# Kernel optimization log

Measured on AMD Instinct MI355X. Metric: run time of the kernel, lower is better.

The kernel has to match this reference:

```python
import jax, jax.numpy as jnp
import numpy as np

NUM_RBF = 16
MAX_REL = 32
TOP_K = 48
RBF_D_MIN, RBF_D_MAX = 2.0, 22.0
CB_A, CB_B, CB_C = -0.58273431, 0.56802827, -0.54067466
LN_EPS = 1e-5


def gather_L(x, idx):
    # x: (B, L, ...)  idx: (B, L, K) -> (B, L, K, ...): neighbors along L per batch
    return jax.vmap(lambda xb, ib: xb[ib])(x, idx)


def rbf_encode(D):
    mu = jnp.linspace(RBF_D_MIN, RBF_D_MAX, NUM_RBF, dtype=D.dtype)  # (16,)
    sigma = (RBF_D_MAX - RBF_D_MIN) / NUM_RBF
    return jnp.exp(-((D[..., None] - mu) / sigma) ** 2)


def setup_inputs() -> dict:
    key = jax.random.key(0)
    ks = jax.random.split(key, 4)
    B, L = 4, 2048
    num_pos, hidden = 16, 128
    X = jax.random.normal(ks[0], (B, L, 4, 3), jnp.float32) * 3.0
    residue_mask = jnp.ones((B, L), jnp.float32)
    R_idx = jnp.tile(jnp.arange(L, dtype=jnp.int32)[None, :], (B, 1))
    chain_labels = jnp.zeros((B, L), jnp.int32)
    W_pos = jax.random.normal(ks[1], (2 * MAX_REL + 2, num_pos), jnp.float32) * 0.1
    b_pos = jnp.zeros((num_pos,), jnp.float32)
    W_edge = jax.random.normal(ks[2], (25 * NUM_RBF + num_pos, hidden), jnp.float32) * 0.05
    ln_gamma = jnp.ones((hidden,), jnp.float32)
    ln_beta = jnp.zeros((hidden,), jnp.float32)
    return dict(X=X, residue_mask=residue_mask, R_idx=R_idx, chain_labels=chain_labels,
                W_pos=W_pos, b_pos=b_pos, W_edge=W_edge, ln_gamma=ln_gamma, ln_beta=ln_beta)


def reference(X, residue_mask, R_idx, chain_labels, W_pos, b_pos, W_edge, ln_gamma, ln_beta):
    B, L = X.shape[:2]
    # virtual CB from N, CA, C
    N, CA, C = X[..., 0, :], X[..., 1, :], X[..., 2, :]
    b = CA - N
    c = C - CA
    a = jnp.cross(b, c)
    CB = CB_A * a + CB_B * b + CB_C * c + CA                      # (B, L, 3)
    atoms_5 = jnp.concatenate([X, CB[:, :, None, :]], axis=-2)    # (B, L, 5, 3)

    # kNN on CA-CA squared distances, masked columns pushed far away
    diff = CA[:, :, None, :] - CA[:, None, :, :]                  # (B, L, L, 3)
    dist_sq = jnp.sum(diff ** 2, axis=-1)
    dist_sq = dist_sq + (1.0 - residue_mask)[:, None, :] * 1e6
    _, E_idx = jax.lax.top_k(-dist_sq, TOP_K)                     # smallest-k -> (B, L, K)

    # 25 atom-pair RBF features
    X_g = gather_L(atoms_5, E_idx)                                # (B, L, K, 5, 3)
    D = jnp.sqrt(jnp.sum((atoms_5[:, :, None, :, None, :]
                          - X_g[:, :, :, None, :, :]) ** 2, axis=-1) + 1e-6)  # (B,L,K,5,5)
    rbf = rbf_encode(D).reshape(B, L, TOP_K, 25 * NUM_RBF)        # (B, L, K, 400)

    # positional encodings (ProteinMPNN style)
    R_g = gather_L(R_idx, E_idx)                                  # (B, L, K)
    C_g = gather_L(chain_labels, E_idx)
    offset = R_idx[:, :, None] - R_g
    same_chain = (chain_labels[:, :, None] == C_g).astype(jnp.int32)
    d = jnp.clip(offset + MAX_REL, 0, 2 * MAX_REL) * same_chain + (1 - same_chain) * (2 * MAX_REL + 1)
    d_onehot = jax.nn.one_hot(d, 2 * MAX_REL + 2, dtype=W_pos.dtype)  # (B, L, K, 66)
    pos_enc = jnp.einsum('blkc,cp->blkp', d_onehot, W_pos) + b_pos    # (B, L, K, 16)

    edge_input = jnp.concatenate([pos_enc, rbf], axis=-1)         # (B, L, K, 416)
    E = jnp.einsum('blkc,ch->blkh', edge_input, W_edge)           # (B, L, K, 128)
    mean = jnp.mean(E, axis=-1, keepdims=True)
    var = jnp.var(E, axis=-1, keepdims=True)
    E = (E - mean) * jax.lax.rsqrt(var + LN_EPS) * ln_gamma + ln_beta
    return E_idx, E
```

## Files before the change

kernel.cpp:

```cpp
#include <hip/hip_runtime.h>
#include <hip/hip_bf16.h>

#define BB 4
#define LL 2048
#define KK 48
#define HH 128
#define CANDCAP 384
#define FSTR 40
#define DLT 1.06666666667f

using bf16x8 = __attribute__((ext_vector_type(8))) short;
using f32x4  = __attribute__((ext_vector_type(4))) float;
using u64x2  = __attribute__((ext_vector_type(2))) unsigned long long;

__global__ __launch_bounds__(256) void pf13_prep_w(
    const float* __restrict__ Wedge, const float* __restrict__ Wpos,
    const float* __restrict__ bpos, short* __restrict__ Wt) {
    int idx = blockIdx.x * 256 + threadIdx.x;
    if (idx >= 16 * 8 * 16 * 32) return;
    int j  = idx & 7;
    int kg = (idx >> 3) & 3;
    int col = (idx >> 5) & 15;
    int nt = (idx >> 9) & 7;
    int kt = idx >> 12;
    int k = kt * 32 + kg * 8 + j;
    int n = nt * 16 + col;
    float v = 0.0f;
    if (kt < 13) {
        if (k < 400) v = Wedge[(size_t)(16 + k) * HH + n];
    } else {
        int d = k - 416;
        if (d < 66) {
            float s = 0.f;
            #pragma unroll
            for (int p = 0; p < 16; ++p)
                s += (Wpos[d * 16 + p] + bpos[p]) * Wedge[p * HH + n];
            v = s;
        }
    }
    __hip_bfloat16 h = __float2bfloat16(v);
    Wt[idx] = *reinterpret_cast<short*>(&h);
}

__global__ __launch_bounds__(256) void pf13_prep_ca(const float* __restrict__ X,
                                                    const float* __restrict__ mask,
                                                    float4* __restrict__ caq) {
    int i = blockIdx.x * 256 + threadIdx.x;
    if (i >= BB * LL) return;
    const float* x = X + (size_t)i * 12;
    float bias = __fmul_rn(1.0f - mask[i], 1.0e6f);
    caq[i] = make_float4(x[3], x[4], x[5], bias);
}

__global__ __launch_bounds__(256, 6) void pf13_main(
    const float* __restrict__ X,
    const int* __restrict__ Ridx, const int* __restrict__ chain,
    const float* __restrict__ gamma, const float* __restrict__ beta,
    const short* __restrict__ Wt, const float4* __restrict__ caq,
    float* __restrict__ outIdx, float* __restrict__ outEdge) {

    const int row = blockIdx.x;
    const int bq = row >> 11, lq = row & (LL - 1);
    const int tid = threadIdx.x;
    const int lane = tid & 63, wid = tid >> 6;
    const float* Xb = X + (size_t)bq * LL * 12;
    const float4* caqb = caq + (size_t)bq * LL;

    __shared__ __align__(16) union {
        int hist[1024];
        unsigned long long cand[CANDCAP];
        float geo[KK * 15 + 16];
    } uA;
    __shared__ float sD[KK * 25];
    __shared__ __align__(16) short sFeat[2][KK * FSTR];
    __shared__ float sGB[2 * HH];
    __shared__ float sPartS[KK][4], sPartSS[KK][4];
    __shared__ float sMean[KK], sInv[KK];
    __shared__ int sSel[KK], sDcode[KK];
    __shared__ int sWsum[4];
    __shared__ int sBstar, sCc;

    if (tid < HH) { sGB[tid * 2] = gamma[tid]; sGB[tid * 2 + 1] = beta[tid]; }

    const float4 sc = caqb[lq];
    float dval[8];
    #pragma unroll
    for (int i = 0; i < 8; ++i) {
        float4 q = caqb[i * 256 + tid];
        float dx = __fadd_rn(sc.x, -q.x);
        float dy = __fadd_rn(sc.y, -q.y);
        float dz = __fadd_rn(sc.z, -q.z);
        float d2 = __fadd_rn(__fadd_rn(__fmul_rn(dx, dx), __fmul_rn(dy, dy)),
                             __fmul_rn(dz, dz));
        dval[i] = __fadd_rn(d2, q.w);
    }

    *reinterpret_cast<int4*>(&uA.hist[tid * 4]) = make_int4(0, 0, 0, 0);
    if (tid == 0) sCc = 0;
    __syncthreads();
    #pragma unroll
    for (int i = 0; i < 8; ++i)
        atomicAdd(&uA.hist[__float_as_uint(dval[i]) >> 22], 1);
    __syncthreads();

    int c0 = uA.hist[tid * 4 + 0];
    int c1 = uA.hist[tid * 4 + 1];
    int c2 = uA.hist[tid * 4 + 2];
    int c3 = uA.hist[tid * 4 + 3];
    int local = c0 + c1 + c2 + c3;
    int v = local;
    #pragma unroll
    for (int off = 1; off < 64; off <<= 1) {
        int o = __shfl_up(v, off, 64);
        if (lane >= off) v += o;
    }
    if (lane == 63) sWsum[wid] = v;
    __syncthreads();
    int woff = 0;
    #pragma unroll
    for (int w2 = 0; w2 < 4; ++w2) if (w2 < wid) woff += sWsum[w2];
    int incl = woff + v, excl = incl - local;
    if (excl < KK && incl >= KK) {
        int cum = excl, b = tid * 4;
        if (cum + c0 >= KK) sBstar = b;
        else { cum += c0;
            if (cum + c1 >= KK) sBstar = b + 1;
            else { cum += c1;
                if (cum + c2 >= KK) sBstar = b + 2;
                else sBstar = b + 3; } }
    }
    __syncthreads();

    int bstar = sBstar;
    #pragma unroll
    for (int i = 0; i < 8; ++i) {
        unsigned int kb = __float_as_uint(dval[i]);
        if ((int)(kb >> 22) <= bstar) {
            int pos = atomicAdd(&sCc, 1);
            if (pos < CANDCAP)
                uA.cand[pos] =
                    ((unsigned long long)kb << 32) | (unsigned)(i * 256 + tid);
        }
    }
    __syncthreads();

    int C = sCc < CANDCAP ? sCc : CANDCAP;
    for (int ci = tid; ci < C; ci += 256) {
        unsigned long long me = uA.cand[ci];
        int rank = 0, j2 = 0;
        int Cv = C & ~7;
        for (; j2 < Cv; j2 += 8) {
            u64x2 q0 = *reinterpret_cast<u64x2*>(&uA.cand[j2]);
            u64x2 q1 = *reinterpret_cast<u64x2*>(&uA.cand[j2 + 2]);
            u64x2 q2 = *reinterpret_cast<u64x2*>(&uA.cand[j2 + 4]);
            u64x2 q3 = *reinterpret_cast<u64x2*>(&uA.cand[j2 + 6]);
            rank += (q0[0] < me) + (q0[1] < me) + (q1[0] < me) + (q1[1] < me)
                  + (q2[0] < me) + (q2[1] < me) + (q3[0] < me) + (q3[1] < me);
        }
        for (; j2 < C; ++j2) rank += (uA.cand[j2] < me) ? 1 : 0;
        if (rank < KK) sSel[rank] = (int)(me & 0xFFFFFFFFu);
    }
    __syncthreads();

    if (tid < KK) outIdx[(size_t)row * KK + tid] = (float)sSel[tid];

    const float KA = -0.58273431f, KB2 = 0.56802827f, KC = -0.54067466f;
    if (tid < KK) {
        int j = sSel[tid];
        const float* x = Xb + (size_t)j * 12;
        float u0 = x[3] - x[0], u1 = x[4] - x[1], u2 = x[5] - x[2];
        float w0 = x[6] - x[3], w1 = x[7] - x[4], w2 = x[8] - x[5];
        float r0 = u1 * w2 - u2 * w1;
        float r1 = u2 * w0 - u0 * w2;
        float r2 = u0 * w1 - u1 * w0;
        float* o = &uA.geo[tid * 15];
        #pragma unroll
        for (int t = 0; t < 12; ++t) o[t] = x[t];
        o[12] = KA * r0 + KB2 * u0 + KC * w0 + x[3];
        o[13] = KA * r1 + KB2 * u1 + KC * w1 + x[4];
        o[14] = KA * r2 + KB2 * u2 + KC * w2 + x[5];
        int offr = Ridx[row] - Ridx[(size_t)bq * LL + j];
        int same = (chain[row] == chain[(size_t)bq * LL + j]);
        int d = offr + 32;
        d = d < 0 ? 0 : (d > 64 ? 64 : d);
        sDcode[tid] = same ? d : 65;
    }
    if (tid == 64) {
        const float* x = Xb + (size_t)lq * 12;
        float u0 = x[3] - x[0], u1 = x[4] - x[1], u2 = x[5] - x[2];
        float w0 = x[6] - x[3], w1 = x[7] - x[4], w2 = x[8] - x[5];
        float r0 = u1 * w2 - u2 * w1;
        float r1 = u2 * w0 - u0 * w2;
        float r2 = u0 * w1 - u1 * w0;
        float* s = &uA.geo[720];
        #pragma unroll
        for (int t = 0; t < 12; ++t) s[t] = x[t];
        s[12] = KA * r0 + KB2 * u0 + KC * w0 + x[3];
        s[13] = KA * r1 + KB2 * u1 + KC * w1 + x[4];
        s[14] = KA * r2 + KB2 * u2 + KC * w2 + x[5];
    }
    __syncthreads();

    for (int idx = tid; idx < KK * 25; idx += 256) {
        int k = idx / 25, pq = idx % 25, p = pq / 5, q = pq % 5;
        float dx = uA.geo[720 + p * 3 + 0] - uA.geo[k * 15 + q * 3 + 0];
        float dy = uA.geo[720 + p * 3 + 1] - uA.geo[k * 15 + q * 3 + 1];
        float dz = uA.geo[720 + p * 3 + 2] - uA.geo[k * 15 + q * 3 + 2];
        sD[idx] = sqrtf(dx * dx + dy * dy + dz * dz + 1e-6f);
    }
    __syncthreads();

    auto feat_compute = [&](int kt, int fb) {
        if (tid < 192) {
            int pair = tid >> 1, half = tid & 1;
            int k = pair >> 1, pq_lo = pair & 1;
            int pq = kt * 2 + pq_lo;
            bf16x8 ov;
            if (pq < 25) {
                float Dv = sD[k * 25 + pq];
                float t0 = (Dv - 2.0f) * 0.8f;
                float tm = __builtin_fmaf(-(float)(half << 3), DLT, t0);
                #pragma unroll
                for (int mi = 0; mi < 8; ++mi) {
                    float val = __expf(-tm * tm);
                    __hip_bfloat16 hb = __float2bfloat16(val);
                    ov[mi] = *reinterpret_cast<short*>(&hb);
                    tm -= DLT;
                }
            } else {
                #pragma unroll
                for (int mi = 0; mi < 8; ++mi) ov[mi] = 0;
            }
            *reinterpret_cast<bf16x8*>(
                &sFeat[fb][k * FSTR + pq_lo * 16 + (half << 3)]) = ov;
        }
    };

    feat_compute(0, 0);
    __syncthreads();

    f32x4 acc[3][2];
    #pragma unroll
    for (int mt = 0; mt < 3; ++mt)
        #pragma unroll
        for (int nb = 0; nb < 2; ++nb) acc[mt][nb] = (f32x4){0.f, 0.f, 0.f, 0.f};
    const int nt0 = wid * 2;
    const int arow = lane & 15, kg = lane >> 4;

    int cur = 0;
    #pragma unroll 1
    for (int kt = 0; kt < 13; ++kt) {
        const short* wp = Wt + (((size_t)(kt * 8 + nt0) * 16 + arow) * 32 + kg * 8);
        bf16x8 b0 = *reinterpret_cast<const bf16x8*>(wp);
        bf16x8 b1 = *reinterpret_cast<const bf16x8*>(wp + 16 * 32);
        if (kt + 1 < 13) feat_compute(kt + 1, cur ^ 1);
        bf16x8 a0 = *reinterpret_cast<const bf16x8*>(&sFeat[cur][(arow     ) * FSTR + kg * 8]);
        bf16x8 a1 = *reinterpret_cast<const bf16x8*>(&sFeat[cur][(arow + 16) * FSTR + kg * 8]);
        bf16x8 a2 = *reinterpret_cast<const bf16x8*>(&sFeat[cur][(arow + 32) * FSTR + kg * 8]);
        acc[0][0] = __builtin_amdgcn_mfma_f32_16x16x32_bf16(a0, b0, acc[0][0], 0, 0, 0);
        acc[1][0] = __builtin_amdgcn_mfma_f32_16x16x32_bf16(a1, b0, acc[1][0], 0, 0, 0);
        acc[2][0] = __builtin_amdgcn_mfma_f32_16x16x32_bf16(a2, b0, acc[2][0], 0, 0, 0);
        acc[0][1] = __builtin_amdgcn_mfma_f32_16x16x32_bf16(a0, b1, acc[0][1], 0, 0, 0);
        acc[1][1] = __builtin_amdgcn_mfma_f32_16x16x32_bf16(a1, b1, acc[1][1], 0, 0, 0);
        acc[2][1] = __builtin_amdgcn_mfma_f32_16x16x32_bf16(a2, b1, acc[2][1], 0, 0, 0);
        if (kt + 1 < 13) { __syncthreads(); cur ^= 1; }
    }

    int dc0 = sDcode[arow], dc1 = sDcode[arow + 16], dc2 = sDcode[arow + 32];
    #pragma unroll 1
    for (int kp = 0; kp < 3; ++kp) {
        int base = kp * 32 + kg * 8;
        bf16x8 a0, a1, a2;
        #pragma unroll
        for (int j = 0; j < 8; ++j) {
            a0[j] = (dc0 == base + j) ? (short)0x3F80 : (short)0;
            a1[j] = (dc1 == base + j) ? (short)0x3F80 : (short)0;
            a2[j] = (dc2 == base + j) ? (short)0x3F80 : (short)0;
        }
        const short* wp = Wt + (((size_t)((13 + kp) * 8 + nt0) * 16 + arow) * 32 + kg * 8);
        bf16x8 b0 = *reinterpret_cast<const bf16x8*>(wp);
        bf16x8 b1 = *reinterpret_cast<const bf16x8*>(wp + 16 * 32);
        acc[0][0] = __builtin_amdgcn_mfma_f32_16x16x32_bf16(a0, b0, acc[0][0], 0, 0, 0);
        acc[1][0] = __builtin_amdgcn_mfma_f32_16x16x32_bf16(a1, b0, acc[1][0], 0, 0, 0);
        acc[2][0] = __builtin_amdgcn_mfma_f32_16x16x32_bf16(a2, b0, acc[2][0], 0, 0, 0);
        acc[0][1] = __builtin_amdgcn_mfma_f32_16x16x32_bf16(a0, b1, acc[0][1], 0, 0, 0);
        acc[1][1] = __builtin_amdgcn_mfma_f32_16x16x32_bf16(a1, b1, acc[1][1], 0, 0, 0);
        acc[2][1] = __builtin_amdgcn_mfma_f32_16x16x32_bf16(a2, b1, acc[2][1], 0, 0, 0);
    }

    #pragma unroll
    for (int mt = 0; mt < 3; ++mt)
        #pragma unroll
        for (int r = 0; r < 4; ++r) {
            float s = acc[mt][0][r] + acc[mt][1][r];
            float ss = acc[mt][0][r] * acc[mt][0][r]
                     + acc[mt][1][r] * acc[mt][1][r];
            s  += __shfl_xor(s, 1, 64);  ss += __shfl_xor(ss, 1, 64);
            s  += __shfl_xor(s, 2, 64);  ss += __shfl_xor(ss, 2, 64);
            s  += __shfl_xor(s, 4, 64);  ss += __shfl_xor(ss, 4, 64);
            s  += __shfl_xor(s, 8, 64);  ss += __shfl_xor(ss, 8, 64);
            if (arow == 0) {
                int e = mt * 16 + kg * 4 + r;
                sPartS[e][wid] = s;
                sPartSS[e][wid] = ss;
            }
        }
    __syncthreads();
    if (tid < KK) {
        float s = sPartS[tid][0] + sPartS[tid][1] + sPartS[tid][2] + sPartS[tid][3];
        float ss = sPartSS[tid][0] + sPartSS[tid][1] + sPartSS[tid][2] + sPartSS[tid][3];
        float mean = s * (1.0f / 128.0f);
        float var = ss * (1.0f / 128.0f) - mean * mean;
        sMean[tid] = mean;
        sInv[tid] = 1.0f / sqrtf(var + 1e-5f);
    }
    __syncthreads();

    const int col0 = nt0 * 16 + arow, col1 = col0 + 16;
    const float g0 = sGB[col0 * 2], be0 = sGB[col0 * 2 + 1];
    const float g1 = sGB[col1 * 2], be1 = sGB[col1 * 2 + 1];
    float* outR = outEdge + (size_t)row * KK * HH;
    #pragma unroll
    for (int mt = 0; mt < 3; ++mt)
        #pragma unroll
        for (int r = 0; r < 4; ++r) {
            int e = mt * 16 + kg * 4 + r;
            float mean = sMean[e], inv = sInv[e];
            outR[(size_t)e * HH + col0] = (acc[mt][0][r] - mean) * inv * g0 + be0;
            outR[(size_t)e * HH + col1] = (acc[mt][1][r] - mean) * inv * g1 + be1;
        }
}

extern "C" void kernel_launch(void* const* d_in, const int* in_sizes, int n_in,
                              void* d_out, int out_size, void* d_ws, size_t ws_size,
                              hipStream_t stream) {
    const float* X     = (const float*)d_in[0];
    const float* mask  = (const float*)d_in[1];
    const int*   Ridx  = (const int*)d_in[2];
    const int*   chain = (const int*)d_in[3];
    const float* Wpos  = (const float*)d_in[4];
    const float* bpos  = (const float*)d_in[5];
    const float* Wedge = (const float*)d_in[6];
    const float* gamma = (const float*)d_in[7];
    const float* beta  = (const float*)d_in[8];

    float* outBase = (float*)d_out;
    float* outIdx  = outBase;
    float* outEdge = outBase + (size_t)BB * LL * KK;

    short*  Wt  = (short*)d_ws;
    float4* caq = (float4*)((char*)d_ws + 16 * 8 * 16 * 32 * 2);

    hipLaunchKernelGGL(pf13_prep_w, dim3(256), dim3(256), 0, stream,
                       Wedge, Wpos, bpos, Wt);
    hipLaunchKernelGGL(pf13_prep_ca, dim3((BB * LL + 255) / 256), dim3(256), 0,
                       stream, X, mask, caq);
    hipLaunchKernelGGL(pf13_main, dim3(BB * LL), dim3(256), 0, stream,
                       X, Ridx, chain, gamma, beta, Wt, caq, outIdx, outEdge);
}
```

Baseline: 141.3 us.

## Double block size to 512 threads and split per-wave MMA work

Raises the main kernel from 256 to 512 threads per row-block. Each thread now handles half as many distances, histogram bins and RBF features, and each wave owns one 16-column N tile instead of two. The RBF exponentials move to exp2 with an incremental quadratic recurrence that replaces the per-value square, and the one-hot A operands are built with shifts instead of per-element compares. This spreads latency-bound per-row work across more waves and cuts per-thread registers, at the cost of more block-wide barrier overhead and an 8-way partial reduction.

```diff
diff --git a/kernel.cpp b/kernel.cpp
--- a/kernel.cpp
+++ b/kernel.cpp
@@ -8,12 +8,17 @@
 #define CANDCAP 384
 #define FSTR 40
 #define DLT 1.06666666667f
+#define L2E 1.44269504089f
+#define D1A 3.07774901f
+#define D1B 1.64147055f
+#define D2C -3.28294110f
 
 using bf16x8 = __attribute__((ext_vector_type(8))) short;
+using bf16x4 = __attribute__((ext_vector_type(4))) short;
 using f32x4  = __attribute__((ext_vector_type(4))) float;
 using u64x2  = __attribute__((ext_vector_type(2))) unsigned long long;
 
-__global__ __launch_bounds__(256) void pf13_prep_w(
+__global__ __launch_bounds__(256) void pf14_prep_w(
     const float* __restrict__ Wedge, const float* __restrict__ Wpos,
     const float* __restrict__ bpos, short* __restrict__ Wt) {
     int idx = blockIdx.x * 256 + threadIdx.x;
@@ -42,7 +47,7 @@
     Wt[idx] = *reinterpret_cast<short*>(&h);
 }
 
-__global__ __launch_bounds__(256) void pf13_prep_ca(const float* __restrict__ X,
+__global__ __launch_bounds__(256) void pf14_prep_ca(const float* __restrict__ X,
                                                     const float* __restrict__ mask,
                                                     float4* __restrict__ caq) {
     int i = blockIdx.x * 256 + threadIdx.x;
@@ -52,7 +57,7 @@
     caq[i] = make_float4(x[3], x[4], x[5], bias);
 }
 
-__global__ __launch_bounds__(256, 6) void pf13_main(
+__global__ __launch_bounds__(512, 8) void pf14_main(
     const float* __restrict__ X,
     const int* __restrict__ Ridx, const int* __restrict__ chain,
     const float* __restrict__ gamma, const float* __restrict__ beta,
@@ -74,19 +79,19 @@
     __shared__ float sD[KK * 25];
     __shared__ __align__(16) short sFeat[2][KK * FSTR];
     __shared__ float sGB[2 * HH];
-    __shared__ float sPartS[KK][4], sPartSS[KK][4];
+    __shared__ __align__(16) float sPartS[KK][8], sPartSS[KK][8];
     __shared__ float sMean[KK], sInv[KK];
     __shared__ int sSel[KK], sDcode[KK];
-    __shared__ int sWsum[4];
+    __shared__ int sWsum[8];
     __shared__ int sBstar, sCc;
 
     if (tid < HH) { sGB[tid * 2] = gamma[tid]; sGB[tid * 2 + 1] = beta[tid]; }
 
     const float4 sc = caqb[lq];
-    float dval[8];
-    #pragma unroll
-    for (int i = 0; i < 8; ++i) {
-        float4 q = caqb[i * 256 + tid];
+    float dval[4];
+    #pragma unroll
+    for (int i = 0; i < 4; ++i) {
+        float4 q = caqb[i * 512 + tid];
         float dx = __fadd_rn(sc.x, -q.x);
         float dy = __fadd_rn(sc.y, -q.y);
         float dz = __fadd_rn(sc.z, -q.z);
@@ -95,19 +100,17 @@
         dval[i] = __fadd_rn(d2, q.w);
     }
 
-    *reinterpret_cast<int4*>(&uA.hist[tid * 4]) = make_int4(0, 0, 0, 0);
+    *reinterpret_cast<int2*>(&uA.hist[tid * 2]) = make_int2(0, 0);
     if (tid == 0) sCc = 0;
     __syncthreads();
     #pragma unroll
-    for (int i = 0; i < 8; ++i)
+    for (int i = 0; i < 4; ++i)
         atomicAdd(&uA.hist[__float_as_uint(dval[i]) >> 22], 1);
     __syncthreads();
 
-    int c0 = uA.hist[tid * 4 + 0];
-    int c1 = uA.hist[tid * 4 + 1];
-    int c2 = uA.hist[tid * 4 + 2];
-    int c3 = uA.hist[tid * 4 + 3];
-    int local = c0 + c1 + c2 + c3;
+    int c0 = uA.hist[tid * 2 + 0];
+    int c1 = uA.hist[tid * 2 + 1];
+    int local = c0 + c1;
     int v = local;
     #pragma unroll
     for (int off = 1; off < 64; off <<= 1) {
@@ -118,34 +121,27 @@
     __syncthreads();
     int woff = 0;
     #pragma unroll
-    for (int w2 = 0; w2 < 4; ++w2) if (w2 < wid) woff += sWsum[w2];
+    for (int w2 = 0; w2 < 8; ++w2) if (w2 < wid) woff += sWsum[w2];
     int incl = woff + v, excl = incl - local;
-    if (excl < KK && incl >= KK) {
-        int cum = excl, b = tid * 4;
-        if (cum + c0 >= KK) sBstar = b;
-        else { cum += c0;
-            if (cum + c1 >= KK) sBstar = b + 1;
-            else { cum += c1;
-                if (cum + c2 >= KK) sBstar = b + 2;
-                else sBstar = b + 3; } }
-    }
+    if (excl < KK && incl >= KK)
+        sBstar = (excl + c0 >= KK) ? tid * 2 : tid * 2 + 1;
     __syncthreads();
 
     int bstar = sBstar;
     #pragma unroll
-    for (int i = 0; i < 8; ++i) {
+    for (int i = 0; i < 4; ++i) {
         unsigned int kb = __float_as_uint(dval[i]);
         if ((int)(kb >> 22) <= bstar) {
             int pos = atomicAdd(&sCc, 1);
             if (pos < CANDCAP)
                 uA.cand[pos] =
-                    ((unsigned long long)kb << 32) | (unsigned)(i * 256 + tid);
+                    ((unsigned long long)kb << 32) | (unsigned)(i * 512 + tid);
         }
     }
     __syncthreads();
 
     int C = sCc < CANDCAP ? sCc : CANDCAP;
-    for (int ci = tid; ci < C; ci += 256) {
+    for (int ci = tid; ci < C; ci += 512) {
         unsigned long long me = uA.cand[ci];
         int rank = 0, j2 = 0;
         int Cv = C & ~7;
@@ -201,7 +197,7 @@
     }
     __syncthreads();
 
-    for (int idx = tid; idx < KK * 25; idx += 256) {
+    for (int idx = tid; idx < KK * 25; idx += 512) {
         int k = idx / 25, pq = idx % 25, p = pq / 5, q = pq % 5;
         float dx = uA.geo[720 + p * 3 + 0] - uA.geo[k * 15 + q * 3 + 0];
         float dy = uA.geo[720 + p * 3 + 1] - uA.geo[k * 15 + q * 3 + 1];
@@ -211,58 +207,53 @@
     __syncthreads();
 
     auto feat_compute = [&](int kt, int fb) {
-        if (tid < 192) {
-            int pair = tid >> 1, half = tid & 1;
+        if (tid < 384) {
+            int q = tid & 3;
+            int pair = tid >> 2;
             int k = pair >> 1, pq_lo = pair & 1;
             int pq = kt * 2 + pq_lo;
-            bf16x8 ov;
+            bf16x4 ov;
             if (pq < 25) {
                 float Dv = sD[k * 25 + pq];
-                float t0 = (Dv - 2.0f) * 0.8f;
-                float tm = __builtin_fmaf(-(float)(half << 3), DLT, t0);
+                float tm = __builtin_fmaf(-(float)(q << 2), DLT, (Dv - 2.0f) * 0.8f);
+                float g  = -(tm * tm) * L2E;
+                float d1 = __builtin_fmaf(D1A, tm, -D1B);
                 #pragma unroll
-                for (int mi = 0; mi < 8; ++mi) {
-                    float val = __expf(-tm * tm);
+                for (int mi = 0; mi < 4; ++mi) {
+                    float val = exp2f(g);
+                    g += d1; d1 += D2C;
                     __hip_bfloat16 hb = __float2bfloat16(val);
                     ov[mi] = *reinterpret_cast<short*>(&hb);
-                    tm -= DLT;
                 }
             } else {
                 #pragma unroll
-                for (int mi = 0; mi < 8; ++mi) ov[mi] = 0;
+                for (int mi = 0; mi < 4; ++mi) ov[mi] = 0;
             }
-            *reinterpret_cast<bf16x8*>(
-                &sFeat[fb][k * FSTR + pq_lo * 16 + (half << 3)]) = ov;
+            *reinterpret_cast<bf16x4*>(
+                &sFeat[fb][k * FSTR + pq_lo * 16 + (q << 2)]) = ov;
         }
     };
 
     feat_compute(0, 0);
     __syncthreads();
 
-    f32x4 acc[3][2];
-    #pragma unroll
-    for (int mt = 0; mt < 3; ++mt)
-        #pragma unroll
-        for (int nb = 0; nb < 2; ++nb) acc[mt][nb] = (f32x4){0.f, 0.f, 0.f, 0.f};
-    const int nt0 = wid * 2;
+    f32x4 acc[3];
+    #pragma unroll
+    for (int mt = 0; mt < 3; ++mt) acc[mt] = (f32x4){0.f, 0.f, 0.f, 0.f};
     const int arow = lane & 15, kg = lane >> 4;
 
     int cur = 0;
     #pragma unroll 1
     for (int kt = 0; kt < 13; ++kt) {
-        const short* wp = Wt + (((size_t)(kt * 8 + nt0) * 16 + arow) * 32 + kg * 8);
+        const short* wp = Wt + (((size_t)(kt * 8 + wid) * 16 + arow) * 32 + kg * 8);
         bf16x8 b0 = *reinterpret_cast<const bf16x8*>(wp);
-        bf16x8 b1 = *reinterpret_cast<const bf16x8*>(wp + 16 * 32);
         if (kt + 1 < 13) feat_compute(kt + 1, cur ^ 1);
         bf16x8 a0 = *reinterpret_cast<const bf16x8*>(&sFeat[cur][(arow     ) * FSTR + kg * 8]);
         bf16x8 a1 = *reinterpret_cast<const bf16x8*>(&sFeat[cur][(arow + 16) * FSTR + kg * 8]);
         bf16x8 a2 = *reinterpret_cast<const bf16x8*>(&sFeat[cur][(arow + 32) * FSTR + kg * 8]);
-        acc[0][0] = __builtin_amdgcn_mfma_f32_16x16x32_bf16(a0, b0, acc[0][0], 0, 0, 0);
-        acc[1][0] = __builtin_amdgcn_mfma_f32_16x16x32_bf16(a1, b0, acc[1][0], 0, 0, 0);
-        acc[2][0] = __builtin_amdgcn_mfma_f32_16x16x32_bf16(a2, b0, acc[2][0], 0, 0, 0);
-        acc[0][1] = __builtin_amdgcn_mfma_f32_16x16x32_bf16(a0, b1, acc[0][1], 0, 0, 0);
-        acc[1][1] = __builtin_amdgcn_mfma_f32_16x16x32_bf16(a1, b1, acc[1][1], 0, 0, 0);
-        acc[2][1] = __builtin_amdgcn_mfma_f32_16x16x32_bf16(a2, b1, acc[2][1], 0, 0, 0);
+        acc[0] = __builtin_amdgcn_mfma_f32_16x16x32_bf16(a0, b0, acc[0], 0, 0, 0);
+        acc[1] = __builtin_amdgcn_mfma_f32_16x16x32_bf16(a1, b0, acc[1], 0, 0, 0);
+        acc[2] = __builtin_amdgcn_mfma_f32_16x16x32_bf16(a2, b0, acc[2], 0, 0, 0);
         if (kt + 1 < 13) { __syncthreads(); cur ^= 1; }
     }
 
@@ -270,31 +261,29 @@
     #pragma unroll 1
     for (int kp = 0; kp < 3; ++kp) {
         int base = kp * 32 + kg * 8;
-        bf16x8 a0, a1, a2;
-        #pragma unroll
-        for (int j = 0; j < 8; ++j) {
-            a0[j] = (dc0 == base + j) ? (short)0x3F80 : (short)0;
-            a1[j] = (dc1 == base + j) ? (short)0x3F80 : (short)0;
-            a2[j] = (dc2 == base + j) ? (short)0x3F80 : (short)0;
-        }
-        const short* wp = Wt + (((size_t)((13 + kp) * 8 + nt0) * 16 + arow) * 32 + kg * 8);
+        union OneHot { unsigned long long u[2]; bf16x8 v; } oh0, oh1, oh2;
+        unsigned int i0 = (unsigned)(dc0 - base);
+        unsigned int i1 = (unsigned)(dc1 - base);
+        unsigned int i2 = (unsigned)(dc2 - base);
+        oh0.u[0] = (i0 < 4) ? (0x3F80ULL << (i0 * 16)) : 0ULL;
+        oh0.u[1] = (i0 - 4 < 4) ? (0x3F80ULL << ((i0 - 4) * 16)) : 0ULL;
+        oh1.u[0] = (i1 < 4) ? (0x3F80ULL << (i1 * 16)) : 0ULL;
+        oh1.u[1] = (i1 - 4 < 4) ? (0x3F80ULL << ((i1 - 4) * 16)) : 0ULL;
+        oh2.u[0] = (i2 < 4) ? (0x3F80ULL << (i2 * 16)) : 0ULL;
+        oh2.u[1] = (i2 - 4 < 4) ? (0x3F80ULL << ((i2 - 4) * 16)) : 0ULL;
+        const short* wp = Wt + (((size_t)((13 + kp) * 8 + wid) * 16 + arow) * 32 + kg * 8);
         bf16x8 b0 = *reinterpret_cast<const bf16x8*>(wp);
-        bf16x8 b1 = *reinterpret_cast<const bf16x8*>(wp + 16 * 32);
-        acc[0][0] = __builtin_amdgcn_mfma_f32_16x16x32_bf16(a0, b0, acc[0][0], 0, 0, 0);
-        acc[1][0] = __builtin_amdgcn_mfma_f32_16x16x32_bf16(a1, b0, acc[1][0], 0, 0, 0);
-        acc[2][0] = __builtin_amdgcn_mfma_f32_16x16x32_bf16(a2, b0, acc[2][0], 0, 0, 0);
-        acc[0][1] = __builtin_amdgcn_mfma_f32_16x16x32_bf16(a0, b1, acc[0][1], 0, 0, 0);
-        acc[1][1] = __builtin_amdgcn_mfma_f32_16x16x32_bf16(a1, b1, acc[1][1], 0, 0, 0);
-        acc[2][1] = __builtin_amdgcn_mfma_f32_16x16x32_bf16(a2, b1, acc[2][1], 0, 0, 0);
+        acc[0] = __builtin_amdgcn_mfma_f32_16x16x32_bf16(oh0.v, b0, acc[0], 0, 0, 0);
+        acc[1] = __builtin_amdgcn_mfma_f32_16x16x32_bf16(oh1.v, b0, acc[1], 0, 0, 0);
+        acc[2] = __builtin_amdgcn_mfma_f32_16x16x32_bf16(oh2.v, b0, acc[2], 0, 0, 0);
     }
 
     #pragma unroll
     for (int mt = 0; mt < 3; ++mt)
         #pragma unroll
         for (int r = 0; r < 4; ++r) {
-            float s = acc[mt][0][r] + acc[mt][1][r];
-            float ss = acc[mt][0][r] * acc[mt][0][r]
-                     + acc[mt][1][r] * acc[mt][1][r];
+            float s = acc[mt][r];
+            float ss = s * s;
             s  += __shfl_xor(s, 1, 64);  ss += __shfl_xor(ss, 1, 64);
             s  += __shfl_xor(s, 2, 64);  ss += __shfl_xor(ss, 2, 64);
             s  += __shfl_xor(s, 4, 64);  ss += __shfl_xor(ss, 4, 64);
@@ -307,8 +296,12 @@
         }
     __syncthreads();
     if (tid < KK) {
-        float s = sPartS[tid][0] + sPartS[tid][1] + sPartS[tid][2] + sPartS[tid][3];
-        float ss = sPartSS[tid][0] + sPartSS[tid][1] + sPartSS[tid][2] + sPartSS[tid][3];
+        f32x4 p0 = *reinterpret_cast<f32x4*>(&sPartS[tid][0]);
+        f32x4 p1 = *reinterpret_cast<f32x4*>(&sPartS[tid][4]);
+        f32x4 q0 = *reinterpret_cast<f32x4*>(&sPartSS[tid][0]);
+        f32x4 q1 = *reinterpret_cast<f32x4*>(&sPartSS[tid][4]);
+        float s = p0[0] + p0[1] + p0[2] + p0[3] + p1[0] + p1[1] + p1[2] + p1[3];
+        float ss = q0[0] + q0[1] + q0[2] + q0[3] + q1[0] + q1[1] + q1[2] + q1[3];
         float mean = s * (1.0f / 128.0f);
         float var = ss * (1.0f / 128.0f) - mean * mean;
         sMean[tid] = mean;
@@ -316,18 +309,16 @@
     }
     __syncthreads();
 
-    const int col0 = nt0 * 16 + arow, col1 = col0 + 16;
-    const float g0 = sGB[col0 * 2], be0 = sGB[col0 * 2 + 1];
-    const float g1 = sGB[col1 * 2], be1 = sGB[col1 * 2 + 1];
+    const int col = wid * 16 + arow;
+    const float g = sGB[col * 2], be = sGB[col * 2 + 1];
     float* outR = outEdge + (size_t)row * KK * HH;
     #pragma unroll
     for (int mt = 0; mt < 3; ++mt)
         #pragma unroll
         for (int r = 0; r < 4; ++r) {
             int e = mt * 16 + kg * 4 + r;
-            float mean = sMean[e], inv = sInv[e];
-            outR[(size_t)e * HH + col0] = (acc[mt][0][r] - mean) * inv * g0 + be0;
-            outR[(size_t)e * HH + col1] = (acc[mt][1][r] - mean) * inv * g1 + be1;
+            outR[(size_t)e * HH + col] =
+                (acc[mt][r] - sMean[e]) * sInv[e] * g + be;
         }
 }
 
@@ -351,10 +342,10 @@
     short*  Wt  = (short*)d_ws;
     float4* caq = (float4*)((char*)d_ws + 16 * 8 * 16 * 32 * 2);
 
-    hipLaunchKernelGGL(pf13_prep_w, dim3(256), dim3(256), 0, stream,
+    hipLaunchKernelGGL(pf14_prep_w, dim3(256), dim3(256), 0, stream,
                        Wedge, Wpos, bpos, Wt);
-    hipLaunchKernelGGL(pf13_prep_ca, dim3((BB * LL + 255) / 256), dim3(256), 0,
+    hipLaunchKernelGGL(pf14_prep_ca, dim3((BB * LL + 255) / 256), dim3(256), 0,
                        stream, X, mask, caq);
-    hipLaunchKernelGGL(pf13_main, dim3(BB * LL), dim3(256), 0, stream,
+    hipLaunchKernelGGL(pf14_main, dim3(BB * LL), dim3(512), 0, stream,
                        X, Ridx, chain, gamma, beta, Wt, caq, outIdx, outEdge);
 }
```

Result: slower. 208.2 us (+47.4%).
